# Kernel tuning notes

Hardware: AMD Instinct MI355X
Metric: run time of the kernel (lower is better)

The kernel has to match this reference:

```python
import jax, jax.numpy as jnp
import numpy as np

MODEL_DIM = 1024
NUM_HEADS = 16
HEAD_DIM = MODEL_DIM // NUM_HEADS
ROPE_BASE = 10000.0


def apply_rope(x):
    # x: [B, H, S, D] -- rotate-half RoPE convention
    S, D = x.shape[-2], x.shape[-1]
    inv_freq = 1.0 / (ROPE_BASE ** (jnp.arange(0, D, 2, dtype=jnp.float32) / D))  # [D/2]
    t = jnp.arange(S, dtype=jnp.float32)
    freqs = t[:, None] * inv_freq[None, :]                  # [S, D/2]
    cos = jnp.concatenate([jnp.cos(freqs), jnp.cos(freqs)], axis=-1)  # [S, D]
    sin = jnp.concatenate([jnp.sin(freqs), jnp.sin(freqs)], axis=-1)
    x1, x2 = x[..., : D // 2], x[..., D // 2 :]
    rot = jnp.concatenate([-x2, x1], axis=-1)
    return x * cos + rot * sin


def setup_inputs() -> dict:
    key = jax.random.key(0)
    k1, k2, k3 = jax.random.split(key, 3)
    B, S, Dm = 4, 2048, MODEL_DIM
    std = 1.0 / np.sqrt(Dm)
    x = jax.random.normal(k1, (B, S, Dm), dtype=jnp.float32)
    w_qkv = jax.random.normal(k2, (Dm, 3 * Dm), dtype=jnp.float32) * std
    b_qkv = jnp.zeros((3 * Dm,), dtype=jnp.float32)
    w_out = jax.random.normal(k3, (Dm, Dm), dtype=jnp.float32) * std
    b_out = jnp.zeros((Dm,), dtype=jnp.float32)
    return {"x": x, "w_qkv": w_qkv, "b_qkv": b_qkv, "w_out": w_out, "b_out": b_out}


def reference(x, w_qkv, b_qkv, w_out, b_out):
    B, S, Dm = x.shape
    H, Dh = NUM_HEADS, HEAD_DIM
    scale = Dh ** -0.5
    qkv = x @ w_qkv + b_qkv                                  # [B, S, 3*Dm]
    qkv = qkv.reshape(B, S, 3, H, Dh).transpose(2, 0, 3, 1, 4)  # [3, B, H, S, Dh]
    q, k, v = qkv[0], qkv[1], qkv[2]
    q = apply_rope(q)
    k = apply_rope(k)
    scores = jnp.einsum("bhqd,bhkd->bhqk", q, k) * scale      # [B, H, S, S]
    causal = jnp.tril(jnp.ones((S, S), dtype=bool))
    scores = jnp.where(causal[None, None], scores, -jnp.inf)
    attn = jax.nn.softmax(scores, axis=-1)
    out = jnp.einsum("bhqk,bhkd->bhqd", attn, v)              # [B, H, S, Dh]
    out = out.transpose(0, 2, 1, 3).reshape(B, S, Dm)
    out = out @ w_out + b_out
    return out, attn
```

## Files before the change

### kernel.cpp

```cpp
#include <hip/hip_runtime.h>
#include <hip/hip_bf16.h>
#include <stdint.h>

typedef unsigned short u16;
typedef __attribute__((ext_vector_type(4))) float f32x4;
typedef __attribute__((ext_vector_type(8))) short s16x8;

#define SEQ 2048
#define NB 4
#define DM 1024
#define NHD 16
#define DH 64

__device__ __forceinline__ u16 f2bf(float f) {
  union { float f; uint32_t u; } v; v.f = f;
  return (u16)((v.u + 0x7FFFu + ((v.u >> 16) & 1u)) >> 16);
}
__device__ __forceinline__ float bf2f(u16 u) {
  union { uint32_t u; float f; } v; v.u = ((uint32_t)u) << 16;
  return v.f;
}
__device__ __forceinline__ void gload16(const u16* g, u16* l) {
  __builtin_amdgcn_global_load_lds((const __attribute__((address_space(1))) void*)g,
                                   (__attribute__((address_space(3))) void*)l, 16, 0, 0);
}

__device__ __forceinline__ void stage64x64_swz(const u16* gbase, long gstride,
                                               u16* lds, int tid) {
  int l = tid & 63, w = tid >> 6;
  int rsub = l >> 3;
  int srcElem = ((l & 7) ^ rsub) * 8;
  #pragma unroll
  for (int p = 0; p < 2; ++p) {
    int row0 = w * 16 + p * 8;
    gload16(gbase + (long)(row0 + rsub) * gstride + srcElem, lds + row0 * 64);
  }
}
__device__ __forceinline__ s16x8 frag_swz(const u16* lds, int row, int cb) {
  return *(const s16x8*)&lds[row * 64 + (cb ^ ((row & 7) << 3))];
}

__global__ __launch_bounds__(256) void k_cvt(const float* __restrict__ in,
                                             u16* __restrict__ out, int n4) {
  int idx = blockIdx.x * 256 + threadIdx.x;
  int stride = gridDim.x * 256;
  for (; idx < n4; idx += stride) {
    float4 v = ((const float4*)in)[idx];
    ushort4 o;
    o.x = f2bf(v.x); o.y = f2bf(v.y); o.z = f2bf(v.z); o.w = f2bf(v.w);
    ((ushort4*)out)[idx] = o;
  }
}

__global__ __launch_bounds__(256) void k_tpose(const float* __restrict__ in,
                                               u16* __restrict__ out, int R, int C) {
  __shared__ u16 tile[64][65];
  int c0 = blockIdx.x * 64, r0 = blockIdx.y * 64;
  int tx = threadIdx.x & 63, ty = threadIdx.x >> 6;
  #pragma unroll
  for (int rr = ty; rr < 64; rr += 4)
    tile[rr][tx] = f2bf(in[(long)(r0 + rr) * C + c0 + tx]);
  __syncthreads();
  #pragma unroll
  for (int cc = ty; cc < 64; cc += 4)
    out[(long)(c0 + cc) * R + r0 + tx] = tile[tx][cc];
}

template<int OUT_BF16>
__global__ __launch_bounds__(256) void k_gemm(const u16* __restrict__ A,
                                              const u16* __restrict__ Bt_g,
                                              const float* __restrict__ bias,
                                              void* __restrict__ Cout,
                                              int M, int N, int K) {
  __shared__ u16 As[128 * 64];
  __shared__ u16 Bs[128 * 64];
  int tid = threadIdx.x, lane = tid & 63, wave = tid >> 6;
  int wm = (wave >> 1) * 64, wn = (wave & 1) * 64;
  long m0 = (long)blockIdx.y * 128, n0 = (long)blockIdx.x * 128;
  int lrow = lane & 15, lk8 = (lane >> 4) * 8;
  int srow = wave * 8 + (lane >> 3);
  int scol = (lane & 7) * 8;
  const u16* Ag = &A[(m0 + srow) * (long)K + scol];
  const u16* Bg = &Bt_g[(n0 + srow) * (long)K + scol];
  f32x4 acc[4][4] = {};
  for (int k0 = 0; k0 < K; k0 += 64) {
    __syncthreads();
    #pragma unroll
    for (int p = 0; p < 4; ++p) {
      gload16(Ag + (long)p * 32 * K + k0, &As[(p * 32 + wave * 8) * 64]);
      gload16(Bg + (long)p * 32 * K + k0, &Bs[(p * 32 + wave * 8) * 64]);
    }
    __syncthreads();
    #pragma unroll
    for (int h = 0; h < 2; ++h) {
      s16x8 af[4], bfr[4];
      #pragma unroll
      for (int t = 0; t < 4; ++t)
        af[t]  = *(const s16x8*)&As[(wm + t * 16 + lrow) * 64 + h * 32 + lk8];
      #pragma unroll
      for (int t = 0; t < 4; ++t)
        bfr[t] = *(const s16x8*)&Bs[(wn + t * 16 + lrow) * 64 + h * 32 + lk8];
      #pragma unroll
      for (int i = 0; i < 4; ++i)
        #pragma unroll
        for (int j = 0; j < 4; ++j)
          acc[i][j] = __builtin_amdgcn_mfma_f32_16x16x32_bf16(af[i], bfr[j], acc[i][j], 0, 0, 0);
    }
  }
  int crow = (lane >> 4) * 4, ccol = lane & 15;
  #pragma unroll
  for (int i = 0; i < 4; ++i)
  #pragma unroll
  for (int j = 0; j < 4; ++j) {
    long col = n0 + wn + j * 16 + ccol;
    float bv = bias ? bias[col] : 0.f;
    #pragma unroll
    for (int r = 0; r < 4; ++r) {
      long row = m0 + wm + i * 16 + crow + r;
      float v = acc[i][j][r] + bv;
      if (OUT_BF16) ((u16*)Cout)[row * N + col] = f2bf(v);
      else          ((float*)Cout)[row * N + col] = v;
    }
  }
}

__global__ __launch_bounds__(256) void k_rope(const u16* __restrict__ qkv,
                                              u16* __restrict__ Qr,
                                              u16* __restrict__ Kr) {
  int t = blockIdx.x * 256 + threadIdx.x;
  int i = t & 31;
  int h = (t >> 5) & 15;
  int s = (t >> 9) & 2047;
  int b = t >> 20;
  long row = ((long)(b * SEQ + s)) * 3072 + h * 64;
  float q1 = bf2f(qkv[row + i]),        q2 = bf2f(qkv[row + i + 32]);
  float k1 = bf2f(qkv[row + 1024 + i]), k2 = bf2f(qkv[row + 1024 + i + 32]);
  float fq = exp2f(-(float)i * 0.4152410118609203f);
  float ang = (float)s * fq;
  float c = cosf(ang), sn = sinf(ang);
  long ob = ((long)((b * NHD + h) * SEQ + s)) * 64;
  Qr[ob + i]      = f2bf((q1 * c - q2 * sn) * 0.125f);
  Qr[ob + i + 32] = f2bf((q2 * c + q1 * sn) * 0.125f);
  Kr[ob + i]      = f2bf(k1 * c - k2 * sn);
  Kr[ob + i + 32] = f2bf(k2 * c + k1 * sn);
}

__global__ __launch_bounds__(256) void k_vt(const u16* __restrict__ qkv,
                                            u16* __restrict__ VtG) {
  __shared__ u16 t[64][65];
  int jt = blockIdx.x, bh = blockIdx.y;
  int b = bh >> 4, h = bh & 15;
  int tid = threadIdx.x;
  int r = tid >> 3, c8 = (tid & 7) * 8;
  long base = ((long)(b * SEQ + jt * 64)) * 3072 + 2048 + h * 64;
  #pragma unroll
  for (int half = 0; half < 2; ++half) {
    s16x8 v = *(const s16x8*)&qkv[base + (long)(r + half * 32) * 3072 + c8];
    #pragma unroll
    for (int j = 0; j < 8; ++j) t[r + half * 32][c8 + j] = (u16)v[j];
  }
  __syncthreads();
  long ob = ((long)bh * 32 + jt) * 4096;
  int d = tid >> 3, r8 = (tid & 7) * 8;
  #pragma unroll
  for (int half = 0; half < 2; ++half) {
    s16x8 o;
    #pragma unroll
    for (int j = 0; j < 8; ++j) o[j] = (short)t[r8 + j][d + half * 32];
    *(s16x8*)&VtG[ob + (long)(d + half * 32) * 64 + r8] = o;
  }
}

__global__ __launch_bounds__(256) void k_attn(const u16* __restrict__ Qr,
                                              const u16* __restrict__ Kr,
                                              const u16* __restrict__ VtG,
                                              float* __restrict__ attn,
                                              u16* __restrict__ ctx) {
  constexpr int LP = 72;
  __shared__ u16 Ks[64 * 64];
  __shared__ u16 Vs[64 * 64];
  __shared__ u16 Ps[4][16 * LP];
  int tid = threadIdx.x, lane = tid & 63, wave = tid >> 6;
  int wgid = blockIdx.x;
  int c = wgid & 7, t7 = wgid >> 3;
  int bh = c * 8 + (t7 >> 5);
  int qb = 31 - (t7 & 31);
  int q0 = qb * 64;
  int qw0 = q0 + wave * 16;
  int lrow = lane & 15, lg = lane >> 4, lk8 = (lane >> 4) * 8;
  const u16* Qb = Qr + (long)bh * SEQ * 64;
  const u16* Kb = Kr + (long)bh * SEQ * 64;
  const u16* Vtb = VtG + (long)bh * 32 * 4096;
  float* attn_bh = attn + (long)bh * SEQ * SEQ;

  s16x8 qf0 = *(const s16x8*)&Qb[(long)(qw0 + lrow) * 64 + lk8];
  s16x8 qf1 = *(const s16x8*)&Qb[(long)(qw0 + lrow) * 64 + 32 + lk8];

  int njt = qb + 1;

  float suml[4] = {0.f, 0.f, 0.f, 0.f};
  for (int jt = 0; jt < njt; ++jt) {
    __syncthreads();
    stage64x64_swz(Kb + (long)jt * 64 * 64, 64, Ks, tid);
    __syncthreads();
    int ctmax = (jt < njt - 1) ? 3 : wave;
    long k0 = (long)jt * 64;
    for (int ct = 0; ct <= ctmax; ++ct) {
      int row = ct * 16 + lrow;
      s16x8 kf0 = frag_swz(Ks, row, lk8);
      s16x8 kf1 = frag_swz(Ks, row, 32 + lk8);
      f32x4 sa = {0.f, 0.f, 0.f, 0.f};
      sa = __builtin_amdgcn_mfma_f32_16x16x32_bf16(qf0, kf0, sa, 0, 0, 0);
      sa = __builtin_amdgcn_mfma_f32_16x16x32_bf16(qf1, kf1, sa, 0, 0, 0);
      bool diag = (jt == njt - 1) && (ct == wave);
      int gcol = (int)k0 + ct * 16 + lrow;
      #pragma unroll
      for (int r = 0; r < 4; ++r) {
        int grow = qw0 + lg * 4 + r;
        float e = (!diag || gcol <= grow) ? __expf(sa[r]) : 0.f;
        suml[r] += e;
      }
    }
  }
  #pragma unroll
  for (int r = 0; r < 4; ++r) {
    float v = suml[r];
    v += __shfl_xor(v, 1, 16);
    v += __shfl_xor(v, 2, 16);
    v += __shfl_xor(v, 4, 16);
    v += __shfl_xor(v, 8, 16);
    suml[r] = 1.0f / v;
  }

  f32x4 oacc[4] = {};
  u16* ps = &Ps[wave][0];
  for (int jt = 0; jt < njt; ++jt) {
    __syncthreads();
    stage64x64_swz(Kb + (long)jt * 64 * 64, 64, Ks, tid);
    stage64x64_swz(Vtb + jt * 4096, 64, Vs, tid);
    __syncthreads();
    int ctmax = (jt < njt - 1) ? 3 : wave;
    long k0 = (long)jt * 64;
    #pragma unroll
    for (int ct = 0; ct < 4; ++ct) {
      if (ct <= ctmax) {
        int row = ct * 16 + lrow;
        s16x8 kf0 = frag_swz(Ks, row, lk8);
        s16x8 kf1 = frag_swz(Ks, row, 32 + lk8);
        f32x4 sa = {0.f, 0.f, 0.f, 0.f};
        sa = __builtin_amdgcn_mfma_f32_16x16x32_bf16(qf0, kf0, sa, 0, 0, 0);
        sa = __builtin_amdgcn_mfma_f32_16x16x32_bf16(qf1, kf1, sa, 0, 0, 0);
        bool diag = (jt == njt - 1) && (ct == wave);
        int gcol = (int)k0 + ct * 16 + lrow;
        #pragma unroll
        for (int r = 0; r < 4; ++r) {
          int grow = qw0 + lg * 4 + r;
          float e = (!diag || gcol <= grow) ? __expf(sa[r]) : 0.f;
          ps[(lg * 4 + r) * LP + ct * 16 + lrow] = f2bf(e * suml[r]);
        }
      } else {
        #pragma unroll
        for (int r = 0; r < 4; ++r)
          ps[(lg * 4 + r) * LP + ct * 16 + lrow] = 0;
      }
    }
    s16x8 pf0 = *(const s16x8*)&ps[lrow * LP + lk8];
    s16x8 pf1 = *(const s16x8*)&ps[lrow * LP + 32 + lk8];
    #pragma unroll
    for (int dt = 0; dt < 4; ++dt) {
      int row = dt * 16 + lrow;
      s16x8 vf0 = frag_swz(Vs, row, lk8);
      s16x8 vf1 = frag_swz(Vs, row, 32 + lk8);
      oacc[dt] = __builtin_amdgcn_mfma_f32_16x16x32_bf16(pf0, vf0, oacc[dt], 0, 0, 0);
      oacc[dt] = __builtin_amdgcn_mfma_f32_16x16x32_bf16(pf1, vf1, oacc[dt], 0, 0, 0);
    }
    #pragma unroll
    for (int it = 0; it < 4; ++it) {
      int prow = it * 4 + (lane >> 4);
      int c4 = lane & 15;
      ushort4 pv = *(const ushort4*)&ps[prow * LP + c4 * 4];
      f32x4 o;
      o.x = bf2f(pv.x); o.y = bf2f(pv.y); o.z = bf2f(pv.z); o.w = bf2f(pv.w);
      __builtin_nontemporal_store(o,
          (f32x4*)&attn_bh[(long)(qw0 + prow) * SEQ + k0 + c4 * 4]);
    }
  }

  {
    int cstart = q0 + 64;
    int zc4 = (SEQ - cstart) >> 2;
    f32x4 z = {0.f, 0.f, 0.f, 0.f};
    for (int row = 0; row < 64; ++row) {
      f32x4* dst = (f32x4*)&attn_bh[(long)(q0 + row) * SEQ + cstart];
      for (int cc = tid; cc < zc4; cc += 256)
        __builtin_nontemporal_store(z, &dst[cc]);
    }
  }

  int b = bh >> 4, h = bh & 15;
  #pragma unroll
  for (int dt = 0; dt < 4; ++dt)
  #pragma unroll
  for (int r = 0; r < 4; ++r) {
    long grow = qw0 + lg * 4 + r;
    long col = h * 64 + dt * 16 + lrow;
    ctx[((long)b * SEQ + grow) * DM + col] = f2bf(oacc[dt][r]);
  }
}

extern "C" void kernel_launch(void* const* d_in, const int* in_sizes, int n_in,
                              void* d_out, int out_size, void* d_ws, size_t ws_size,
                              hipStream_t stream) {
  const float* x     = (const float*)d_in[0];
  const float* w_qkv = (const float*)d_in[1];
  const float* b_qkv = (const float*)d_in[2];
  const float* w_out = (const float*)d_in[3];
  const float* b_out = (const float*)d_in[4];
  float* outp = (float*)d_out;
  float* attn = outp + (long)NB * SEQ * DM;

  char* ws = (char*)d_ws;
  u16* Qr  = (u16*)(ws);
  u16* Kr  = (u16*)(ws + 16777216L);
  u16* VtG = (u16*)(ws + 33554432L);
  u16* ctx = (u16*)(ws + 50331648L);
  u16* WoT = (u16*)(ws + 67108864L);

  u16* qkvb = (u16*)attn;
  u16* Xb   = (u16*)((char*)attn + 50331648L);
  u16* WqT  = (u16*)((char*)attn + 67108864L);

  k_cvt<<<1024, 256, 0, stream>>>(x, Xb, (NB * SEQ * DM) / 4);
  k_tpose<<<dim3(3 * DM / 64, DM / 64), 256, 0, stream>>>(w_qkv, WqT, DM, 3 * DM);
  k_tpose<<<dim3(DM / 64, DM / 64), 256, 0, stream>>>(w_out, WoT, DM, DM);

  k_gemm<1><<<dim3(3 * DM / 128, NB * SEQ / 128), 256, 0, stream>>>(
      Xb, WqT, b_qkv, qkvb, NB * SEQ, 3 * DM, DM);

  k_rope<<<(NB * SEQ * NHD * 32) / 256, 256, 0, stream>>>(qkvb, Qr, Kr);
  k_vt<<<dim3(SEQ / 64, NB * NHD), 256, 0, stream>>>(qkvb, VtG);

  k_attn<<<2048, 256, 0, stream>>>(Qr, Kr, VtG, attn, ctx);

  k_gemm<0><<<dim3(DM / 128, NB * SEQ / 128), 256, 0, stream>>>(
      ctx, WoT, b_out, outp, NB * SEQ, DM, DM);
}
```

Measured before the change: 398.6 us.

## Fuse RoPE and V transpose into QKV GEMM epilogue, double-buffer K in attention

Adds a dedicated QKV GEMM whose epilogue applies bias, RoPE and the query scale and writes Q/K head-major and V pre-transposed. This removes the separate rope and V-transpose kernels and the round trip through the intermediate qkv buffer. The first attention pass now double-buffers K tiles across the Ks/Vs shared arrays to overlap loads with compute. In the second pass the attention-probability stores are moved ahead of the PV MFMAs. The epilogue now computes sin/cos per element and uses scattered 2-byte stores, which may be less efficient than the old elementwise kernel.

```diff
diff --git a/kernel.cpp b/kernel.cpp
--- a/kernel.cpp
+++ b/kernel.cpp
@@ -64,6 +64,98 @@
   #pragma unroll
   for (int cc = ty; cc < 64; cc += 4)
     out[(long)(c0 + cc) * R + r0 + tx] = tile[tx][cc];
+}
+
+__global__ __launch_bounds__(256) void k_gemm_qkv(const u16* __restrict__ A,
+                                                  const u16* __restrict__ Bt,
+                                                  const float* __restrict__ bias,
+                                                  u16* __restrict__ Qr,
+                                                  u16* __restrict__ Kr,
+                                                  u16* __restrict__ VtG) {
+  const int K = DM;
+  __shared__ u16 As[128 * 64];
+  __shared__ u16 Bs[128 * 64];
+  int tid = threadIdx.x, lane = tid & 63, wave = tid >> 6;
+  int wm = (wave >> 1) * 64, wn = (wave & 1) * 64;
+  long m0 = (long)blockIdx.y * 128, n0 = (long)blockIdx.x * 128;
+  int lrow = lane & 15, lk8 = (lane >> 4) * 8;
+  int srow = wave * 8 + (lane >> 3);
+  int scol = (lane & 7) * 8;
+  const u16* Ag = &A[(m0 + srow) * (long)K + scol];
+  const u16* Bg = &Bt[(n0 + srow) * (long)K + scol];
+  f32x4 acc[4][4] = {};
+  for (int k0 = 0; k0 < K; k0 += 64) {
+    __syncthreads();
+    #pragma unroll
+    for (int p = 0; p < 4; ++p) {
+      gload16(Ag + (long)p * 32 * K + k0, &As[(p * 32 + wave * 8) * 64]);
+      gload16(Bg + (long)p * 32 * K + k0, &Bs[(p * 32 + wave * 8) * 64]);
+    }
+    __syncthreads();
+    #pragma unroll
+    for (int h = 0; h < 2; ++h) {
+      s16x8 af[4], bfr[4];
+      #pragma unroll
+      for (int t = 0; t < 4; ++t)
+        af[t]  = *(const s16x8*)&As[(wm + t * 16 + lrow) * 64 + h * 32 + lk8];
+      #pragma unroll
+      for (int t = 0; t < 4; ++t)
+        bfr[t] = *(const s16x8*)&Bs[(wn + t * 16 + lrow) * 64 + h * 32 + lk8];
+      #pragma unroll
+      for (int i = 0; i < 4; ++i)
+        #pragma unroll
+        for (int j = 0; j < 4; ++j)
+          acc[i][j] = __builtin_amdgcn_mfma_f32_16x16x32_bf16(af[i], bfr[j], acc[i][j], 0, 0, 0);
+    }
+  }
+  int coln = (int)(n0) + wn;
+  int sec = coln >> 10;
+  int hh = (coln & 1023) >> 6;
+  int crow = (lane >> 4) * 4, ccol = lane & 15;
+  int rowb = (int)m0 + wm;
+  if (sec < 2) {
+    u16* dst = (sec == 0) ? Qr : Kr;
+    float sc = (sec == 0) ? 0.125f : 1.0f;
+    #pragma unroll
+    for (int j2 = 0; j2 < 2; ++j2) {
+      int ih = j2 * 16 + ccol;
+      float fq = exp2f(-(float)ih * 0.4152410118609203f);
+      float bv1 = bias[coln + j2 * 16 + ccol];
+      float bv2 = bias[coln + j2 * 16 + ccol + 32];
+      #pragma unroll
+      for (int i = 0; i < 4; ++i) {
+        #pragma unroll
+        for (int r = 0; r < 4; ++r) {
+          int row = rowb + i * 16 + crow + r;
+          int b = row >> 11, s = row & 2047;
+          float ang = (float)s * fq;
+          float c = cosf(ang), sn = sinf(ang);
+          float v1 = acc[i][j2][r] + bv1;
+          float v2 = acc[i][j2 + 2][r] + bv2;
+          long ob = ((long)((b * NHD + hh) * SEQ + s)) * 64;
+          dst[ob + ih]      = f2bf((v1 * c - v2 * sn) * sc);
+          dst[ob + ih + 32] = f2bf((v2 * c + v1 * sn) * sc);
+        }
+      }
+    }
+  } else {
+    #pragma unroll
+    for (int i = 0; i < 4; ++i) {
+      int row = rowb + i * 16 + crow;
+      int b = row >> 11, sl = row & 2047;
+      int jt = sl >> 6, sr = sl & 63;
+      #pragma unroll
+      for (int j = 0; j < 4; ++j) {
+        int d = j * 16 + ccol;
+        float bv = bias[coln + j * 16 + ccol];
+        long idx = (((long)(b * NHD + hh) * 32 + jt) * 64 + d) * 64 + sr;
+        ushort4 o;
+        o.x = f2bf(acc[i][j][0] + bv); o.y = f2bf(acc[i][j][1] + bv);
+        o.z = f2bf(acc[i][j][2] + bv); o.w = f2bf(acc[i][j][3] + bv);
+        *(ushort4*)&VtG[idx] = o;
+      }
+    }
+  }
 }
 
 template<int OUT_BF16>
@@ -121,53 +213,6 @@
       if (OUT_BF16) ((u16*)Cout)[row * N + col] = f2bf(v);
       else          ((float*)Cout)[row * N + col] = v;
     }
-  }
-}
-
-__global__ __launch_bounds__(256) void k_rope(const u16* __restrict__ qkv,
-                                              u16* __restrict__ Qr,
-                                              u16* __restrict__ Kr) {
-  int t = blockIdx.x * 256 + threadIdx.x;
-  int i = t & 31;
-  int h = (t >> 5) & 15;
-  int s = (t >> 9) & 2047;
-  int b = t >> 20;
-  long row = ((long)(b * SEQ + s)) * 3072 + h * 64;
-  float q1 = bf2f(qkv[row + i]),        q2 = bf2f(qkv[row + i + 32]);
-  float k1 = bf2f(qkv[row + 1024 + i]), k2 = bf2f(qkv[row + 1024 + i + 32]);
-  float fq = exp2f(-(float)i * 0.4152410118609203f);
-  float ang = (float)s * fq;
-  float c = cosf(ang), sn = sinf(ang);
-  long ob = ((long)((b * NHD + h) * SEQ + s)) * 64;
-  Qr[ob + i]      = f2bf((q1 * c - q2 * sn) * 0.125f);
-  Qr[ob + i + 32] = f2bf((q2 * c + q1 * sn) * 0.125f);
-  Kr[ob + i]      = f2bf(k1 * c - k2 * sn);
-  Kr[ob + i + 32] = f2bf(k2 * c + k1 * sn);
-}
-
-__global__ __launch_bounds__(256) void k_vt(const u16* __restrict__ qkv,
-                                            u16* __restrict__ VtG) {
-  __shared__ u16 t[64][65];
-  int jt = blockIdx.x, bh = blockIdx.y;
-  int b = bh >> 4, h = bh & 15;
-  int tid = threadIdx.x;
-  int r = tid >> 3, c8 = (tid & 7) * 8;
-  long base = ((long)(b * SEQ + jt * 64)) * 3072 + 2048 + h * 64;
-  #pragma unroll
-  for (int half = 0; half < 2; ++half) {
-    s16x8 v = *(const s16x8*)&qkv[base + (long)(r + half * 32) * 3072 + c8];
-    #pragma unroll
-    for (int j = 0; j < 8; ++j) t[r + half * 32][c8 + j] = (u16)v[j];
-  }
-  __syncthreads();
-  long ob = ((long)bh * 32 + jt) * 4096;
-  int d = tid >> 3, r8 = (tid & 7) * 8;
-  #pragma unroll
-  for (int half = 0; half < 2; ++half) {
-    s16x8 o;
-    #pragma unroll
-    for (int j = 0; j < 8; ++j) o[j] = (short)t[r8 + j][d + half * 32];
-    *(s16x8*)&VtG[ob + (long)(d + half * 32) * 64 + r8] = o;
   }
 }
 
@@ -199,16 +244,19 @@
   int njt = qb + 1;
 
   float suml[4] = {0.f, 0.f, 0.f, 0.f};
+  stage64x64_swz(Kb, 64, Ks, tid);
+  __syncthreads();
   for (int jt = 0; jt < njt; ++jt) {
-    __syncthreads();
-    stage64x64_swz(Kb + (long)jt * 64 * 64, 64, Ks, tid);
-    __syncthreads();
+    const u16* cur = (jt & 1) ? Vs : Ks;
+    u16* nxt = (jt & 1) ? Ks : Vs;
+    if (jt + 1 < njt)
+      stage64x64_swz(Kb + (long)(jt + 1) * 64 * 64, 64, nxt, tid);
     int ctmax = (jt < njt - 1) ? 3 : wave;
     long k0 = (long)jt * 64;
     for (int ct = 0; ct <= ctmax; ++ct) {
       int row = ct * 16 + lrow;
-      s16x8 kf0 = frag_swz(Ks, row, lk8);
-      s16x8 kf1 = frag_swz(Ks, row, 32 + lk8);
+      s16x8 kf0 = frag_swz(cur, row, lk8);
+      s16x8 kf1 = frag_swz(cur, row, 32 + lk8);
       f32x4 sa = {0.f, 0.f, 0.f, 0.f};
       sa = __builtin_amdgcn_mfma_f32_16x16x32_bf16(qf0, kf0, sa, 0, 0, 0);
       sa = __builtin_amdgcn_mfma_f32_16x16x32_bf16(qf1, kf1, sa, 0, 0, 0);
@@ -221,6 +269,7 @@
         suml[r] += e;
       }
     }
+    __syncthreads();
   }
   #pragma unroll
   for (int r = 0; r < 4; ++r) {
@@ -264,16 +313,6 @@
           ps[(lg * 4 + r) * LP + ct * 16 + lrow] = 0;
       }
     }
-    s16x8 pf0 = *(const s16x8*)&ps[lrow * LP + lk8];
-    s16x8 pf1 = *(const s16x8*)&ps[lrow * LP + 32 + lk8];
-    #pragma unroll
-    for (int dt = 0; dt < 4; ++dt) {
-      int row = dt * 16 + lrow;
-      s16x8 vf0 = frag_swz(Vs, row, lk8);
-      s16x8 vf1 = frag_swz(Vs, row, 32 + lk8);
-      oacc[dt] = __builtin_amdgcn_mfma_f32_16x16x32_bf16(pf0, vf0, oacc[dt], 0, 0, 0);
-      oacc[dt] = __builtin_amdgcn_mfma_f32_16x16x32_bf16(pf1, vf1, oacc[dt], 0, 0, 0);
-    }
     #pragma unroll
     for (int it = 0; it < 4; ++it) {
       int prow = it * 4 + (lane >> 4);
@@ -283,6 +322,16 @@
       o.x = bf2f(pv.x); o.y = bf2f(pv.y); o.z = bf2f(pv.z); o.w = bf2f(pv.w);
       __builtin_nontemporal_store(o,
           (f32x4*)&attn_bh[(long)(qw0 + prow) * SEQ + k0 + c4 * 4]);
+    }
+    s16x8 pf0 = *(const s16x8*)&ps[lrow * LP + lk8];
+    s16x8 pf1 = *(const s16x8*)&ps[lrow * LP + 32 + lk8];
+    #pragma unroll
+    for (int dt = 0; dt < 4; ++dt) {
+      int row = dt * 16 + lrow;
+      s16x8 vf0 = frag_swz(Vs, row, lk8);
+      s16x8 vf1 = frag_swz(Vs, row, 32 + lk8);
+      oacc[dt] = __builtin_amdgcn_mfma_f32_16x16x32_bf16(pf0, vf0, oacc[dt], 0, 0, 0);
+      oacc[dt] = __builtin_amdgcn_mfma_f32_16x16x32_bf16(pf1, vf1, oacc[dt], 0, 0, 0);
     }
   }
 
@@ -326,19 +375,15 @@
   u16* ctx = (u16*)(ws + 50331648L);
   u16* WoT = (u16*)(ws + 67108864L);
 
-  u16* qkvb = (u16*)attn;
-  u16* Xb   = (u16*)((char*)attn + 50331648L);
-  u16* WqT  = (u16*)((char*)attn + 67108864L);
+  u16* Xb  = (u16*)attn;
+  u16* WqT = (u16*)((char*)attn + 16777216L);
 
   k_cvt<<<1024, 256, 0, stream>>>(x, Xb, (NB * SEQ * DM) / 4);
   k_tpose<<<dim3(3 * DM / 64, DM / 64), 256, 0, stream>>>(w_qkv, WqT, DM, 3 * DM);
   k_tpose<<<dim3(DM / 64, DM / 64), 256, 0, stream>>>(w_out, WoT, DM, DM);
 
-  k_gemm<1><<<dim3(3 * DM / 128, NB * SEQ / 128), 256, 0, stream>>>(
-      Xb, WqT, b_qkv, qkvb, NB * SEQ, 3 * DM, DM);
-
-  k_rope<<<(NB * SEQ * NHD * 32) / 256, 256, 0, stream>>>(qkvb, Qr, Kr);
-  k_vt<<<dim3(SEQ / 64, NB * NHD), 256, 0, stream>>>(qkvb, VtG);
+  k_gemm_qkv<<<dim3(3 * DM / 128, NB * SEQ / 128), 256, 0, stream>>>(
+      Xb, WqT, b_qkv, Qr, Kr, VtG);
 
   k_attn<<<2048, 256, 0, stream>>>(Qr, Kr, VtG, attn, ctx);
 
```

After: 861.9 us. 2.16x slower.
